# Optimization experiments

Measured on AMD Instinct MI355X. Metric: run time of the kernel, lower is better.

Reference implementation:

```python
import jax, jax.numpy as jnp
import numpy as np

D_MODEL = 1024
N_HEAD = 16
HEAD_DIM = D_MODEL // N_HEAD


def setup_inputs() -> dict:
    key = jax.random.key(0)
    ks = jax.random.split(key, 9)
    B, S, D = 2, 2048, D_MODEL
    s = 1.0 / np.sqrt(D)
    return {
        "x": jax.random.normal(ks[0], (B, S, D), dtype=jnp.float32),
        "Wq": jax.random.normal(ks[1], (D, D), dtype=jnp.float32) * s,
        "bq": jnp.zeros((D,), dtype=jnp.float32),
        "Wk": jax.random.normal(ks[2], (D, D), dtype=jnp.float32) * s,
        "bk": jnp.zeros((D,), dtype=jnp.float32),
        "Wv": jax.random.normal(ks[3], (D, D), dtype=jnp.float32) * s,
        "bv": jnp.zeros((D,), dtype=jnp.float32),
        "Wo": jax.random.normal(ks[4], (D, D), dtype=jnp.float32) * s,
        "bo": jnp.zeros((D,), dtype=jnp.float32),
    }


def _split_heads(t):
    B, S, D = t.shape
    return t.reshape(B, S, N_HEAD, HEAD_DIM).transpose(0, 2, 1, 3)  # [B,H,S,d]


def reference(x, Wq, bq, Wk, bk, Wv, bv, Wo, bo):
    B, S, D = x.shape
    q = _split_heads(x @ Wq + bq)
    k = _split_heads(x @ Wk + bk)
    v = _split_heads(x @ Wv + bv)
    present = jnp.stack((k, v))  # [2,B,H,S,d]
    # NOTE: module scales by sqrt(d_model), not sqrt(head_dim)
    scores = jnp.einsum("bhqd,bhkd->bhqk", q, k) / jnp.sqrt(jnp.float32(D_MODEL))
    causal = jnp.tril(jnp.ones((S, S), dtype=bool))
    scores = jnp.where(causal, scores, -jnp.inf)
    probs = jax.nn.softmax(scores, axis=-1)
    attn = jnp.einsum("bhqk,bhkd->bhqd", probs, v)
    attn = attn.transpose(0, 2, 1, 3).reshape(B, S, D)
    out = attn @ Wo + bo
    return out, present
```

## Files before the change

### kernel.cpp

```cpp
#include <hip/hip_runtime.h>
#include <hip/hip_bf16.h>

typedef __attribute__((ext_vector_type(8))) short short8;
typedef __attribute__((ext_vector_type(4))) short short4v;
typedef __attribute__((ext_vector_type(4))) float f32x4;

#define S_LEN 2048
#define DM 1024
#define NH 16
#define HD 64

__device__ __forceinline__ short f2b(float f) {
    __hip_bfloat16 h = __float2bfloat16(f);
    return *reinterpret_cast<short*>(&h);
}

__global__ void k_convert_x(const float* __restrict__ x, short* __restrict__ Af) {
    int t = blockIdx.x * 256 + threadIdx.x;
    int s = t >> 7, kc = t & 127;
    const float* xp = x + (size_t)s * DM + kc * 8;
    f32x4 v0 = *reinterpret_cast<const f32x4*>(xp);
    f32x4 v1 = *reinterpret_cast<const f32x4*>(xp + 4);
    short8 o;
    for (int e = 0; e < 4; e++) { o[e] = f2b(v0[e]); o[4 + e] = f2b(v1[e]); }
    int R = s >> 6, m = (s >> 4) & 3, lr = s & 15;
    int kstep = kc >> 3, ks = (kc >> 2) & 1, lg = kc & 3;
    size_t off = ((((size_t)(R * 16 + kstep) * 2 + ks) * 4 + m) * 64 + lg * 16 + lr) * 8;
    *reinterpret_cast<short8*>(Af + off) = o;
}

__global__ void k_transpose_w4(const float* __restrict__ W0, const float* __restrict__ W1,
                               const float* __restrict__ W2, const float* __restrict__ W3,
                               short* __restrict__ T0, short* __restrict__ T1,
                               short* __restrict__ T2, short* __restrict__ T3) {
    __shared__ float tile[32][33];
    const int z = blockIdx.z;
    const float* W = (z == 0) ? W0 : (z == 1) ? W1 : (z == 2) ? W2 : W3;
    short* Wt = (z == 0) ? T0 : (z == 1) ? T1 : (z == 2) ? T2 : T3;
    int tx = threadIdx.x, ty = threadIdx.y;
    int nb = blockIdx.x * 32, kb = blockIdx.y * 32;
    for (int i = 0; i < 4; i++)
        tile[ty + i * 8][tx] = W[(size_t)(kb + ty + i * 8) * DM + nb + tx];
    __syncthreads();
    if (ty < 4) {
        int col = nb + tx;
        int k0 = kb + ty * 8;
        short8 o;
#pragma unroll
        for (int e = 0; e < 8; e++) o[e] = f2b(tile[ty * 8 + e][tx]);
        int C = col >> 6, n = (col >> 4) & 3, lr = col & 15;
        int kstep = k0 >> 6, ksb = (k0 >> 5) & 1, lg = (k0 >> 3) & 3;
        *reinterpret_cast<short8*>(
            &Wt[((((size_t)(C * 16 + kstep) * 2 + ksb) * 4 + n) * 64 + lg * 16 + lr) * 8]) = o;
    }
}

__global__ __launch_bounds__(64) void k_gemm_qkv(
    const short* __restrict__ Af,
    const short* __restrict__ Bq, const short* __restrict__ Bk, const short* __restrict__ Bv,
    const float* __restrict__ bq, const float* __restrict__ bk, const float* __restrict__ bv,
    short* __restrict__ Qb, short* __restrict__ Kfrag, short* __restrict__ Vfrag,
    float* __restrict__ pK, float* __restrict__ pV)
{
    const int bid = blockIdx.x;
    const unsigned orig = (bid & 7) * 384 + (bid >> 3);
    const int R = orig / 48;
    const int rem = orig - R * 48;
    const int z = rem >> 4, C = rem & 15;
    const short* Bf = (z == 0) ? Bq : (z == 1) ? Bk : Bv;
    const float* bias = (z == 0) ? bq : (z == 1) ? bk : bv;
    const int l = threadIdx.x;
    const int lr = l & 15, lg = l >> 4;

    f32x4 acc[4][4];
#pragma unroll
    for (int m = 0; m < 4; m++)
#pragma unroll
        for (int n = 0; n < 4; n++) acc[m][n] = (f32x4)0.0f;

    const short* ap = Af + (size_t)R * 16 * 4096 + l * 8;
    const short* bp = Bf + (size_t)C * 16 * 4096 + l * 8;

#pragma unroll 1
    for (int kstep = 0; kstep < 16; ++kstep) {
        short8 a[2][4], b[2][4];
#pragma unroll
        for (int ks = 0; ks < 2; ks++)
#pragma unroll
            for (int i = 0; i < 4; i++) {
                a[ks][i] = *reinterpret_cast<const short8*>(ap + (ks * 4 + i) * 512);
                b[ks][i] = *reinterpret_cast<const short8*>(bp + (ks * 4 + i) * 512);
            }
        ap += 4096; bp += 4096;
#pragma unroll
        for (int ks = 0; ks < 2; ks++)
#pragma unroll
            for (int m = 0; m < 4; m++)
#pragma unroll
                for (int n = 0; n < 4; n++)
                    acc[m][n] = __builtin_amdgcn_mfma_f32_16x16x32_bf16(a[ks][m], b[ks][n], acc[m][n], 0, 0, 0);
    }

    for (int m = 0; m < 4; m++)
        for (int n = 0; n < 4; n++) {
            int row = R * 64 + m * 16 + lg * 4;
            int col = C * 64 + n * 16 + lr;
            float bv_ = bias[col];
            int b_ = row >> 11, sI0 = row & 2047, hI = col >> 6, dh = col & 63;
            if (z == 0) {
                for (int r = 0; r < 4; r++) {
                    float v = acc[m][n][r] + bv_;
                    Qb[(size_t)(row + r) * DM + col] = f2b(v * 0.0450842200575152f);
                }
            } else if (z == 1) {
                for (int r = 0; r < 4; r++) {
                    float v = acc[m][n][r] + bv_;
                    int sI = sI0 + r;
                    pK[(((size_t)(b_ * NH + hI)) * S_LEN + sI) * HD + dh] = v;
                    int j = sI >> 6, kk = sI & 63;
                    int cg = ((kk >> 4) & 2) | ((kk >> 2) & 1);
                    int lrA = ((kk >> 3) & 3) * 4 + (kk & 3);
                    int lane = lrA + ((dh >> 3) & 3) * 16;
                    int ks = dh >> 5, e = dh & 7;
                    Kfrag[((((size_t)(b_ * NH + hI) * 32 + j) * 2 + ks) * 4 + cg) * 512
                          + lane * 8 + e] = f2b(v);
                }
            } else {
                int j = sI0 >> 6, ks = (sI0 >> 5) & 1;
                int dg = dh >> 4;
                int lane = (dh & 15) + ((sI0 >> 3) & 3) * 16;
                int e0 = sI0 & 7;
                short4v tv;
                for (int r = 0; r < 4; r++) {
                    float v = acc[m][n][r] + bv_;
                    pV[(((size_t)(b_ * NH + hI)) * S_LEN + (sI0 + r)) * HD + dh] = v;
                    tv[r] = f2b(v);
                }
                *reinterpret_cast<short4v*>(
                    &Vfrag[((((size_t)(b_ * NH + hI) * 32 + j) * 2 + ks) * 4 + dg) * 512
                           + lane * 8 + e0]) = tv;
            }
        }
}

__global__ __launch_bounds__(64) void k_gemm_o(
    const short* __restrict__ Af, const short* __restrict__ Bf,
    const float* __restrict__ bo, float* __restrict__ out)
{
    const int bid = blockIdx.x;
    const int orig = (bid & 7) * 128 + (bid >> 3);
    const int R = orig >> 4, C = orig & 15;
    const int l = threadIdx.x;
    const int lr = l & 15, lg = l >> 4;

    f32x4 acc[4][4];
#pragma unroll
    for (int m = 0; m < 4; m++)
#pragma unroll
        for (int n = 0; n < 4; n++) acc[m][n] = (f32x4)0.0f;

    const short* ap = Af + (size_t)R * 16 * 4096 + l * 8;
    const short* bp = Bf + (size_t)C * 16 * 4096 + l * 8;

#pragma unroll 1
    for (int kstep = 0; kstep < 16; ++kstep) {
        short8 a[2][4], b[2][4];
#pragma unroll
        for (int ks = 0; ks < 2; ks++)
#pragma unroll
            for (int i = 0; i < 4; i++) {
                a[ks][i] = *reinterpret_cast<const short8*>(ap + (ks * 4 + i) * 512);
                b[ks][i] = *reinterpret_cast<const short8*>(bp + (ks * 4 + i) * 512);
            }
        ap += 4096; bp += 4096;
#pragma unroll
        for (int ks = 0; ks < 2; ks++)
#pragma unroll
            for (int m = 0; m < 4; m++)
#pragma unroll
                for (int n = 0; n < 4; n++)
                    acc[m][n] = __builtin_amdgcn_mfma_f32_16x16x32_bf16(a[ks][m], b[ks][n], acc[m][n], 0, 0, 0);
    }
    for (int m = 0; m < 4; m++)
        for (int n = 0; n < 4; n++) {
            int row = R * 64 + m * 16 + lg * 4;
            int col = C * 64 + n * 16 + lr;
            float bv_ = bo[col];
            for (int r = 0; r < 4; r++)
                out[(size_t)(row + r) * DM + col] = acc[m][n][r] + bv_;
        }
}

__global__ __launch_bounds__(64) void k_attn(
    const short* __restrict__ Qb, const short* __restrict__ Kfrag,
    const short* __restrict__ Vfrag, short* __restrict__ Afo)
{
    const int bid = blockIdx.x;
    const int orig = (bid & 7) * 512 + (bid >> 3);
    const int bh = orig >> 7;
    const int strip = 127 - (orig & 127);
    const int h = bh & 15, b = bh >> 4;
    const int l = threadIdx.x;
    const int lr = l & 15, lg = l >> 4;
    const short* Qp = Qb + (size_t)b * S_LEN * DM + (size_t)h * HD;
    const short* Kbh = Kfrag + (size_t)bh * 32 * 4096;
    const short* Vbh = Vfrag + (size_t)bh * 32 * 4096;

    const int jmax = strip >> 2;
    const int qrow = strip * 16 + lr;
    short8 qf0 = *reinterpret_cast<const short8*>(Qp + (size_t)qrow * DM + lg * 8);
    short8 qf1 = *reinterpret_cast<const short8*>(Qp + (size_t)qrow * DM + 32 + lg * 8);
    f32x4 o[4];
#pragma unroll
    for (int dg = 0; dg < 4; dg++) o[dg] = (f32x4)0.0f;
    float lrun = 0.0f;

    const short* kp = Kbh + l * 8;
    const short* vp = Vbh + l * 8;
    short8 kc[2][4], vc[2][4];
#pragma unroll
    for (int ks = 0; ks < 2; ks++)
#pragma unroll
        for (int cg = 0; cg < 4; cg++) {
            kc[ks][cg] = *reinterpret_cast<const short8*>(kp + (ks * 4 + cg) * 512);
            vc[ks][cg] = *reinterpret_cast<const short8*>(vp + (ks * 4 + cg) * 512);
        }

    for (int j = 0; j <= jmax; ++j) {
        f32x4 s[4];
#pragma unroll
        for (int cg = 0; cg < 4; cg++) s[cg] = (f32x4)0.0f;
#pragma unroll
        for (int ks = 0; ks < 2; ks++) {
            const short8 qf = ks ? qf1 : qf0;
#pragma unroll
            for (int cg = 0; cg < 4; cg++)
                s[cg] = __builtin_amdgcn_mfma_f32_16x16x32_bf16(kc[ks][cg], qf, s[cg], 0, 0, 0);
        }
        if (j < jmax) {
            kp += 4096;
#pragma unroll
            for (int ks = 0; ks < 2; ks++)
#pragma unroll
                for (int cg = 0; cg < 4; cg++)
                    kc[ks][cg] = *reinterpret_cast<const short8*>(kp + (ks * 4 + cg) * 512);
        }
        if (j == jmax) {
#pragma unroll
            for (int cg = 0; cg < 4; cg++)
#pragma unroll
                for (int r = 0; r < 4; r++) {
                    int n = ((cg >> 1) << 5) + (lg << 3) + ((cg & 1) << 2) + r;
                    if (j * 64 + n > qrow) s[cg][r] = -INFINITY;
                }
        }
        float rs = 0.0f;
#pragma unroll
        for (int cg = 0; cg < 4; cg++)
#pragma unroll
            for (int r = 0; r < 4; r++) {
                float p = __builtin_amdgcn_exp2f(s[cg][r]);
                s[cg][r] = p;
                rs += p;
            }
        lrun += rs;
        short8 pf0, pf1;
#pragma unroll
        for (int r = 0; r < 4; r++) {
            pf0[r] = f2b(s[0][r]); pf0[4 + r] = f2b(s[1][r]);
            pf1[r] = f2b(s[2][r]); pf1[4 + r] = f2b(s[3][r]);
        }
#pragma unroll
        for (int ks = 0; ks < 2; ks++) {
            const short8 pf = ks ? pf1 : pf0;
#pragma unroll
            for (int dg = 0; dg < 4; dg++)
                o[dg] = __builtin_amdgcn_mfma_f32_16x16x32_bf16(vc[ks][dg], pf, o[dg], 0, 0, 0);
        }
        if (j < jmax) {
            vp += 4096;
#pragma unroll
            for (int ks = 0; ks < 2; ks++)
#pragma unroll
                for (int cg = 0; cg < 4; cg++)
                    vc[ks][cg] = *reinterpret_cast<const short8*>(vp + (ks * 4 + cg) * 512);
        }
    }
    lrun += __shfl_xor(lrun, 16);
    lrun += __shfl_xor(lrun, 32);
    float rinv = 1.0f / lrun;
    const size_t Ro = (size_t)(b * 32 + (strip >> 2));
    const int mo = strip & 3;
#pragma unroll
    for (int dg = 0; dg < 4; dg++) {
        short4v ov;
#pragma unroll
        for (int r = 0; r < 4; r++) ov[r] = f2b(o[dg][r] * rinv);
        int lane_o = ((dg & 1) * 2 + (lg >> 1)) * 16 + lr;
        size_t off = (((Ro * 16 + h) * 2 + (dg >> 1)) * 4 + mo) * 512
                     + (size_t)lane_o * 8 + (lg & 1) * 4;
        *reinterpret_cast<short4v*>(Afo + off) = ov;
    }
}

extern "C" void kernel_launch(void* const* d_in, const int* in_sizes, int n_in,
                              void* d_out, int out_size, void* d_ws, size_t ws_size,
                              hipStream_t stream) {
    const float* x  = (const float*)d_in[0];
    const float* Wq = (const float*)d_in[1];
    const float* bq = (const float*)d_in[2];
    const float* Wk = (const float*)d_in[3];
    const float* bk = (const float*)d_in[4];
    const float* Wv = (const float*)d_in[5];
    const float* bv = (const float*)d_in[6];
    const float* Wo = (const float*)d_in[7];
    const float* bo = (const float*)d_in[8];

    float* out = (float*)d_out;
    float* presentK = out + (size_t)4194304;
    float* presentV = presentK + (size_t)4194304;

    char* ws = (char*)d_ws;
    short* Af    = (short*)(ws);
    short* Bfq   = (short*)(ws + ((size_t)8  << 20));
    short* Bfk   = (short*)(ws + ((size_t)10 << 20));
    short* Bfv   = (short*)(ws + ((size_t)12 << 20));
    short* Bfo   = (short*)(ws + ((size_t)14 << 20));
    short* Qb    = (short*)(ws + ((size_t)16 << 20));
    short* Kfrag = (short*)(ws + ((size_t)24 << 20));
    short* Vfrag = (short*)(ws + ((size_t)32 << 20));
    short* Afo   = (short*)(ws + ((size_t)40 << 20));

    k_convert_x<<<dim3(2048), dim3(256), 0, stream>>>(x, Af);
    k_transpose_w4<<<dim3(32, 32, 4), dim3(32, 8), 0, stream>>>(
        Wq, Wk, Wv, Wo, Bfq, Bfk, Bfv, Bfo);
    k_gemm_qkv<<<dim3(3072), dim3(64), 0, stream>>>(
        Af, Bfq, Bfk, Bfv, bq, bk, bv, Qb, Kfrag, Vfrag, presentK, presentV);
    k_attn<<<dim3(4096), dim3(64), 0, stream>>>(Qb, Kfrag, Vfrag, Afo);
    k_gemm_o<<<dim3(1024), dim3(64), 0, stream>>>(Afo, Bfo, bo, out);
}
```

Before: 119.6 us.

## Process two query strips per attention wavefront to reuse K/V fragments

Each attention block now handles two adjacent 16-row query strips, sharing the K and V fragment loads across both and issuing twice the MFMAs per loaded tile. The grid is halved to 2048 blocks. This is meant to cut redundant global K/V traffic and load latency per MFMA. In exchange it raises register pressure, which may lower occupancy, and gives coarser load balancing across blocks.

```diff
diff --git a/kernel.cpp b/kernel.cpp
--- a/kernel.cpp
+++ b/kernel.cpp
@@ -196,9 +196,9 @@
     const short* __restrict__ Vfrag, short* __restrict__ Afo)
 {
     const int bid = blockIdx.x;
-    const int orig = (bid & 7) * 512 + (bid >> 3);
-    const int bh = orig >> 7;
-    const int strip = 127 - (orig & 127);
+    const int orig = (bid & 7) * 256 + (bid >> 3);
+    const int bh = orig >> 6;
+    const int p = 63 - (orig & 63);
     const int h = bh & 15, b = bh >> 4;
     const int l = threadIdx.x;
     const int lr = l & 15, lg = l >> 4;
@@ -206,14 +206,17 @@
     const short* Kbh = Kfrag + (size_t)bh * 32 * 4096;
     const short* Vbh = Vfrag + (size_t)bh * 32 * 4096;
 
-    const int jmax = strip >> 2;
-    const int qrow = strip * 16 + lr;
-    short8 qf0 = *reinterpret_cast<const short8*>(Qp + (size_t)qrow * DM + lg * 8);
-    short8 qf1 = *reinterpret_cast<const short8*>(Qp + (size_t)qrow * DM + 32 + lg * 8);
-    f32x4 o[4];
-#pragma unroll
-    for (int dg = 0; dg < 4; dg++) o[dg] = (f32x4)0.0f;
-    float lrun = 0.0f;
+    const int jmax = p >> 1;
+    const int sA = 2 * p, sB = 2 * p + 1;
+    const int qrowA = sA * 16 + lr, qrowB = sB * 16 + lr;
+    short8 qfA0 = *reinterpret_cast<const short8*>(Qp + (size_t)qrowA * DM + lg * 8);
+    short8 qfA1 = *reinterpret_cast<const short8*>(Qp + (size_t)qrowA * DM + 32 + lg * 8);
+    short8 qfB0 = *reinterpret_cast<const short8*>(Qp + (size_t)qrowB * DM + lg * 8);
+    short8 qfB1 = *reinterpret_cast<const short8*>(Qp + (size_t)qrowB * DM + 32 + lg * 8);
+    f32x4 oA[4], oB[4];
+#pragma unroll
+    for (int dg = 0; dg < 4; dg++) { oA[dg] = (f32x4)0.0f; oB[dg] = (f32x4)0.0f; }
+    float lrunA = 0.0f, lrunB = 0.0f;
 
     const short* kp = Kbh + l * 8;
     const short* vp = Vbh + l * 8;
@@ -227,15 +230,18 @@
         }
 
     for (int j = 0; j <= jmax; ++j) {
-        f32x4 s[4];
-#pragma unroll
-        for (int cg = 0; cg < 4; cg++) s[cg] = (f32x4)0.0f;
+        f32x4 sAcc[4], sBcc[4];
+#pragma unroll
+        for (int cg = 0; cg < 4; cg++) { sAcc[cg] = (f32x4)0.0f; sBcc[cg] = (f32x4)0.0f; }
 #pragma unroll
         for (int ks = 0; ks < 2; ks++) {
-            const short8 qf = ks ? qf1 : qf0;
-#pragma unroll
-            for (int cg = 0; cg < 4; cg++)
-                s[cg] = __builtin_amdgcn_mfma_f32_16x16x32_bf16(kc[ks][cg], qf, s[cg], 0, 0, 0);
+            const short8 qfa = ks ? qfA1 : qfA0;
+            const short8 qfb = ks ? qfB1 : qfB0;
+#pragma unroll
+            for (int cg = 0; cg < 4; cg++) {
+                sAcc[cg] = __builtin_amdgcn_mfma_f32_16x16x32_bf16(kc[ks][cg], qfa, sAcc[cg], 0, 0, 0);
+                sBcc[cg] = __builtin_amdgcn_mfma_f32_16x16x32_bf16(kc[ks][cg], qfb, sBcc[cg], 0, 0, 0);
+            }
         }
         if (j < jmax) {
             kp += 4096;
@@ -251,31 +257,38 @@
 #pragma unroll
                 for (int r = 0; r < 4; r++) {
                     int n = ((cg >> 1) << 5) + (lg << 3) + ((cg & 1) << 2) + r;
-                    if (j * 64 + n > qrow) s[cg][r] = -INFINITY;
+                    if (j * 64 + n > qrowA) sAcc[cg][r] = -INFINITY;
+                    if (j * 64 + n > qrowB) sBcc[cg][r] = -INFINITY;
                 }
         }
-        float rs = 0.0f;
+        float rsA = 0.0f, rsB = 0.0f;
 #pragma unroll
         for (int cg = 0; cg < 4; cg++)
 #pragma unroll
             for (int r = 0; r < 4; r++) {
-                float p = __builtin_amdgcn_exp2f(s[cg][r]);
-                s[cg][r] = p;
-                rs += p;
-            }
-        lrun += rs;
-        short8 pf0, pf1;
+                float pa = __builtin_amdgcn_exp2f(sAcc[cg][r]);
+                float pb = __builtin_amdgcn_exp2f(sBcc[cg][r]);
+                sAcc[cg][r] = pa; sBcc[cg][r] = pb;
+                rsA += pa; rsB += pb;
+            }
+        lrunA += rsA; lrunB += rsB;
+        short8 pfA0, pfA1, pfB0, pfB1;
 #pragma unroll
         for (int r = 0; r < 4; r++) {
-            pf0[r] = f2b(s[0][r]); pf0[4 + r] = f2b(s[1][r]);
-            pf1[r] = f2b(s[2][r]); pf1[4 + r] = f2b(s[3][r]);
+            pfA0[r] = f2b(sAcc[0][r]); pfA0[4 + r] = f2b(sAcc[1][r]);
+            pfA1[r] = f2b(sAcc[2][r]); pfA1[4 + r] = f2b(sAcc[3][r]);
+            pfB0[r] = f2b(sBcc[0][r]); pfB0[4 + r] = f2b(sBcc[1][r]);
+            pfB1[r] = f2b(sBcc[2][r]); pfB1[4 + r] = f2b(sBcc[3][r]);
         }
 #pragma unroll
         for (int ks = 0; ks < 2; ks++) {
-            const short8 pf = ks ? pf1 : pf0;
-#pragma unroll
-            for (int dg = 0; dg < 4; dg++)
-                o[dg] = __builtin_amdgcn_mfma_f32_16x16x32_bf16(vc[ks][dg], pf, o[dg], 0, 0, 0);
+            const short8 pfa = ks ? pfA1 : pfA0;
+            const short8 pfb = ks ? pfB1 : pfB0;
+#pragma unroll
+            for (int dg = 0; dg < 4; dg++) {
+                oA[dg] = __builtin_amdgcn_mfma_f32_16x16x32_bf16(vc[ks][dg], pfa, oA[dg], 0, 0, 0);
+                oB[dg] = __builtin_amdgcn_mfma_f32_16x16x32_bf16(vc[ks][dg], pfb, oB[dg], 0, 0, 0);
+            }
         }
         if (j < jmax) {
             vp += 4096;
@@ -286,20 +299,26 @@
                     vc[ks][cg] = *reinterpret_cast<const short8*>(vp + (ks * 4 + cg) * 512);
         }
     }
-    lrun += __shfl_xor(lrun, 16);
-    lrun += __shfl_xor(lrun, 32);
-    float rinv = 1.0f / lrun;
-    const size_t Ro = (size_t)(b * 32 + (strip >> 2));
-    const int mo = strip & 3;
+    lrunA += __shfl_xor(lrunA, 16); lrunA += __shfl_xor(lrunA, 32);
+    lrunB += __shfl_xor(lrunB, 16); lrunB += __shfl_xor(lrunB, 32);
+    float rinvA = 1.0f / lrunA, rinvB = 1.0f / lrunB;
+    const size_t RoA = (size_t)(b * 32 + (sA >> 2));
+    const int moA = sA & 3, moB = sB & 3;
 #pragma unroll
     for (int dg = 0; dg < 4; dg++) {
-        short4v ov;
-#pragma unroll
-        for (int r = 0; r < 4; r++) ov[r] = f2b(o[dg][r] * rinv);
+        short4v ovA, ovB;
+#pragma unroll
+        for (int r = 0; r < 4; r++) {
+            ovA[r] = f2b(oA[dg][r] * rinvA);
+            ovB[r] = f2b(oB[dg][r] * rinvB);
+        }
         int lane_o = ((dg & 1) * 2 + (lg >> 1)) * 16 + lr;
-        size_t off = (((Ro * 16 + h) * 2 + (dg >> 1)) * 4 + mo) * 512
-                     + (size_t)lane_o * 8 + (lg & 1) * 4;
-        *reinterpret_cast<short4v*>(Afo + off) = ov;
+        size_t offA = (((RoA * 16 + h) * 2 + (dg >> 1)) * 4 + moA) * 512
+                      + (size_t)lane_o * 8 + (lg & 1) * 4;
+        size_t offB = (((RoA * 16 + h) * 2 + (dg >> 1)) * 4 + moB) * 512
+                      + (size_t)lane_o * 8 + (lg & 1) * 4;
+        *reinterpret_cast<short4v*>(Afo + offA) = ovA;
+        *reinterpret_cast<short4v*>(Afo + offB) = ovB;
     }
 }
 
@@ -336,6 +355,6 @@
         Wq, Wk, Wv, Wo, Bfq, Bfk, Bfv, Bfo);
     k_gemm_qkv<<<dim3(3072), dim3(64), 0, stream>>>(
         Af, Bfq, Bfk, Bfv, bq, bk, bv, Qb, Kfrag, Vfrag, presentK, presentV);
-    k_attn<<<dim3(4096), dim3(64), 0, stream>>>(Qb, Kfrag, Vfrag, Afo);
+    k_attn<<<dim3(2048), dim3(64), 0, stream>>>(Qb, Kfrag, Vfrag, Afo);
     k_gemm_o<<<dim3(1024), dim3(64), 0, stream>>>(Afo, Bfo, bo, out);
 }
```

Result: faster. 116.6 us (-2.5%).
